# Optimization experiments

Measured on AMD Instinct MI355X. Metric: run time of the kernel, lower is better.

Reference implementation:

```python
import jax, jax.numpy as jnp
import numpy as np

N = 524288   # number of (column, layer) samples
NCH = 30     # n_channel, fixed by the hard-coded filter vectors

# Per-gas channel filters for (h2o, o3, co2, u, n2o, ch4), each length 30.
FILTERS = jnp.array([
    [1,1,1,1,1,1,1,1,1,1,1,1,1,1,1,1,1,1,1,1,1,1,0,0,0,0,0,0,1,1],  # h2o
    [1,1,0,0,0,0,0,0,0,0,0,0,0,0,0,0,1,1,1,1,1,1,0,0,1,1,1,1,1,1],  # o3
    [1,1,0,0,1,1,0,0,1,1,0,0,1,1,0,0,0,0,0,0,0,0,0,0,0,0,0,0,1,1],  # co2
    [1,1,0,0,0,0,0,0,0,0,0,0,0,0,1,1,1,1,1,1,1,1,0,0,0,0,1,1,1,1],  # u
    [1,1,0,0,1,0,0,0,0,0,0,0,0,0,0,0,0,0,0,0,0,0,0,0,0,0,0,0,1,1],  # n2o
    [1,1,1,1,0,0,1,1,0,0,1,1,0,0,0,0,0,0,0,0,0,0,0,0,0,0,0,0,1,1],  # ch4
], dtype=jnp.float32)


def setup_inputs() -> dict:
    key = jax.random.key(0)
    ks = jax.random.split(key, 11)
    u = lambda k, shape, lo, hi: jax.random.uniform(k, shape, jnp.float32, lo, hi)
    return {
        "tpl": jax.random.normal(ks[0], (N, 3), jnp.float32),   # temp, pressure, log_pressure
        "cons": jax.random.uniform(ks[1], (N, 8), jnp.float32), # constituent masses
        # eight Linear(1, 30, bias=False) weights (lw, iw, h2o, o3, co2, u, n2o, ch4)
        "w_gas": u(ks[2], (8, NCH), -0.9, 0.5),
        # six ke-MLPs (2 -> 6 -> 4 -> 4 -> 1), stacked over gas axis g=6
        "ke_W1": u(ks[3], (6, 6, 2), -0.1, 0.1),
        "ke_b1": u(ks[4], (6, 6), 0.9, 1.1),
        "ke_W2": u(ks[5], (6, 4, 6), -0.1, 0.1),
        "ke_b2": u(ks[6], (6, 4), 0.9, 1.1),
        "ke_W3": u(ks[7], (6, 4, 4), -0.1, 0.1),
        "ke_b3": u(ks[8], (6, 4), 0.9, 1.1),
        "ke_Wo": u(ks[9], (6, 4), -0.1, 0.1),
        "ke_bo": u(ks[10], (6,), -0.1, 0.1),
    }


def reference(tpl, cons, w_gas, ke_W1, ke_b1, ke_W2, ke_b2, ke_W3, ke_b3, ke_Wo, ke_bo):
    t_p = tpl[:, :2]                                             # [N,2]
    # six tiny MLPs, vectorized over gas axis g (dropout is identity at eval)
    h = jax.nn.relu(jnp.einsum('ghi,ni->gnh', ke_W1, t_p) + ke_b1[:, None, :])   # [6,N,6]
    h = jax.nn.relu(jnp.einsum('goh,gnh->gno', ke_W2, h) + ke_b2[:, None, :])    # [6,N,4]
    h = jax.nn.relu(jnp.einsum('gph,gnh->gnp', ke_W3, h) + ke_b3[:, None, :])    # [6,N,4]
    s = jax.nn.sigmoid(jnp.einsum('gp,gnp->gn', ke_Wo, h) + ke_bo[:, None])      # [6,N]

    # net_gas(one) == weight vector; exp(w_gas) gives per-channel extinction coeffs
    tau_base = cons[:, None, :] * jnp.exp(w_gas).T[None, :, :]                   # [N,30,8]
    # channel filter * sigmoid modulation for the 6 gas species (slots 2..7)
    mod_gas = (FILTERS[:, None, :] * s[:, :, None]).transpose(1, 2, 0)           # [N,30,6]
    mod = jnp.concatenate(
        [jnp.ones((tpl.shape[0], NCH, 2), tau_base.dtype), mod_gas], axis=2)     # [N,30,8]
    return tau_base * mod                                                        # [N,30,8]
```

## Files before the change

kernel.cpp:

```cpp
#include <hip/hip_runtime.h>
#include <hip/hip_bf16.h>

#define NCHAN 30

__constant__ int FMASK_C[NCHAN] = {63,63,33,33,21,5,33,33,5,5,33,33,5,5,9,9,
                                   11,11,11,11,11,11,0,0,2,2,10,10,63,63};

typedef float f32x4 __attribute__((ext_vector_type(4)));

__global__ __launch_bounds__(256) void ext_kernel(
    const float* __restrict__ tpl,
    const float* __restrict__ cons,
    const float* __restrict__ w_gas,
    const float* __restrict__ W1, const float* __restrict__ b1,
    const float* __restrict__ W2, const float* __restrict__ b2,
    const float* __restrict__ W3, const float* __restrict__ b3,
    const float* __restrict__ Wo, const float* __restrict__ bo,
    f32x4* __restrict__ out4)
{
    __shared__ float p_lds[256][8];
    __shared__ float E_lds[32][8];

    const int tid = threadIdx.x;
    const int n   = blockIdx.x * 256 + tid;

    if (tid < 8 * NCHAN) {
        const int c = tid >> 3, k = tid & 7;
        float e = __expf(w_gas[k * NCHAN + c]);
        if (k >= 2 && !((FMASK_C[c] >> (k - 2)) & 1)) e = 0.f;
        E_lds[c][k] = e;
    }

    const float4* c4 = (const float4*)cons;
    const float4 ca = c4[(size_t)n * 2];
    const float4 cb = c4[(size_t)n * 2 + 1];
    const float t0 = tpl[(size_t)n * 3 + 0];
    const float t1 = tpl[(size_t)n * 3 + 1];

    float s[6];
    #pragma unroll
    for (int g = 0; g < 6; ++g) {
        float h1[6], h2[4], h3[4];
        #pragma unroll
        for (int j = 0; j < 6; ++j)
            h1[j] = fmaxf(0.f, fmaf(W1[g*12 + j*2], t0,
                           fmaf(W1[g*12 + j*2 + 1], t1, b1[g*6 + j])));
        #pragma unroll
        for (int o = 0; o < 4; ++o) {
            float a = b2[g*4 + o];
            #pragma unroll
            for (int j = 0; j < 6; ++j) a = fmaf(W2[g*24 + o*6 + j], h1[j], a);
            h2[o] = fmaxf(0.f, a);
        }
        #pragma unroll
        for (int p = 0; p < 4; ++p) {
            float a = b3[g*4 + p];
            #pragma unroll
            for (int o = 0; o < 4; ++o) a = fmaf(W3[g*16 + p*4 + o], h2[o], a);
            h3[p] = fmaxf(0.f, a);
        }
        float a = bo[g];
        #pragma unroll
        for (int p = 0; p < 4; ++p) a = fmaf(Wo[g*4 + p], h3[p], a);
        s[g] = __fdividef(1.f, 1.f + __expf(-a));
    }

    float4 pa, pb;
    pa.x = ca.x;        pa.y = ca.y;
    pa.z = ca.z * s[0]; pa.w = ca.w * s[1];
    pb.x = cb.x * s[2]; pb.y = cb.y * s[3];
    pb.z = cb.z * s[4]; pb.w = cb.w * s[5];
    *(float4*)&p_lds[tid][0] = pa;
    *(float4*)&p_lds[tid][4] = pb;

    __syncthreads();

    const size_t gbase = (size_t)blockIdx.x * (256 * NCHAN * 2);
    #pragma unroll 6
    for (int i = 0; i < 60; ++i) {
        const unsigned ch  = (unsigned)(i * 256 + tid);
        const unsigned nl  = ch / 60u;
        const unsigned rem = ch - nl * 60u;
        const unsigned c   = rem >> 1;
        const unsigned hi4 = (rem & 1u) << 2;

        const float4 pv = *(const float4*)&p_lds[nl][hi4];
        const float4 ev = *(const float4*)&E_lds[c][hi4];

        f32x4 v;
        v.x = pv.x * ev.x;
        v.y = pv.y * ev.y;
        v.z = pv.z * ev.z;
        v.w = pv.w * ev.w;
        __builtin_nontemporal_store(v, &out4[gbase + ch]);
    }
}

extern "C" void kernel_launch(void* const* d_in, const int* in_sizes, int n_in,
                              void* d_out, int out_size, void* d_ws, size_t ws_size,
                              hipStream_t stream) {
    const float* tpl  = (const float*)d_in[0];
    const float* cons = (const float*)d_in[1];
    const float* wgas = (const float*)d_in[2];
    const float* W1   = (const float*)d_in[3];
    const float* b1   = (const float*)d_in[4];
    const float* W2   = (const float*)d_in[5];
    const float* b2   = (const float*)d_in[6];
    const float* W3   = (const float*)d_in[7];
    const float* b3   = (const float*)d_in[8];
    const float* Wo   = (const float*)d_in[9];
    const float* bo   = (const float*)d_in[10];

    const int nrows = in_sizes[0] / 3;
    const int blocks = nrows / 256;

    ext_kernel<<<dim3(blocks), dim3(256), 0, stream>>>(
        tpl, cons, wgas, W1, b1, W2, b2, W3, b3, Wo, bo, (f32x4*)d_out);
}
```

Baseline: 105.4 us.

## Split fused kernel into MLP pass and separate output-emit pass via workspace

Splits the single fused kernel into two launches. The first computes the per-row modulated constituent vector and the extinction table and writes them to a global workspace. The second reads them back and writes the expanded output. The apparent intent is to separate the compute-heavy MLP phase from the store-bound output phase so each kernel gets better occupancy and no block barrier. The cost is an extra launch and a global-memory round trip of 32 bytes per row.

```diff
diff --git a/kernel.cpp b/kernel.cpp
--- a/kernel.cpp
+++ b/kernel.cpp
@@ -1,5 +1,4 @@
 #include <hip/hip_runtime.h>
-#include <hip/hip_bf16.h>
 
 #define NCHAN 30
 
@@ -8,7 +7,9 @@
 
 typedef float f32x4 __attribute__((ext_vector_type(4)));
 
-__global__ __launch_bounds__(256) void ext_kernel(
+#define WS_P_OFF_F4 64
+
+__global__ __launch_bounds__(256) void mlp_kernel(
     const float* __restrict__ tpl,
     const float* __restrict__ cons,
     const float* __restrict__ w_gas,
@@ -16,19 +17,16 @@
     const float* __restrict__ W2, const float* __restrict__ b2,
     const float* __restrict__ W3, const float* __restrict__ b3,
     const float* __restrict__ Wo, const float* __restrict__ bo,
-    f32x4* __restrict__ out4)
+    float* __restrict__ ws)
 {
-    __shared__ float p_lds[256][8];
-    __shared__ float E_lds[32][8];
-
     const int tid = threadIdx.x;
     const int n   = blockIdx.x * 256 + tid;
 
-    if (tid < 8 * NCHAN) {
+    if (blockIdx.x == 0 && tid < 8 * NCHAN) {
         const int c = tid >> 3, k = tid & 7;
         float e = __expf(w_gas[k * NCHAN + c]);
         if (k >= 2 && !((FMASK_C[c] >> (k - 2)) & 1)) e = 0.f;
-        E_lds[c][k] = e;
+        ws[tid] = e;
     }
 
     const float4* c4 = (const float4*)cons;
@@ -70,22 +68,31 @@
     pa.z = ca.z * s[0]; pa.w = ca.w * s[1];
     pb.x = cb.x * s[2]; pb.y = cb.y * s[3];
     pb.z = cb.z * s[4]; pb.w = cb.w * s[5];
-    *(float4*)&p_lds[tid][0] = pa;
-    *(float4*)&p_lds[tid][4] = pb;
 
-    __syncthreads();
+    float4* p4 = (float4*)ws + WS_P_OFF_F4;
+    p4[(size_t)n * 2]     = pa;
+    p4[(size_t)n * 2 + 1] = pb;
+}
 
-    const size_t gbase = (size_t)blockIdx.x * (256 * NCHAN * 2);
+__global__ __launch_bounds__(256) void emit_kernel(
+    const float* __restrict__ ws,
+    f32x4* __restrict__ out4)
+{
+    const int tid = threadIdx.x;
+    const float4* E4 = (const float4*)ws;
+    const float4* p4 = (const float4*)ws + WS_P_OFF_F4;
+
+    const unsigned rowbase = blockIdx.x * 256u;
+    const size_t   gbase   = (size_t)blockIdx.x * (256 * NCHAN * 2);
+
     #pragma unroll 6
     for (int i = 0; i < 60; ++i) {
         const unsigned ch  = (unsigned)(i * 256 + tid);
         const unsigned nl  = ch / 60u;
         const unsigned rem = ch - nl * 60u;
-        const unsigned c   = rem >> 1;
-        const unsigned hi4 = (rem & 1u) << 2;
 
-        const float4 pv = *(const float4*)&p_lds[nl][hi4];
-        const float4 ev = *(const float4*)&E_lds[c][hi4];
+        const float4 pv = p4[(size_t)(rowbase + nl) * 2 + (rem & 1u)];
+        const float4 ev = E4[rem];
 
         f32x4 v;
         v.x = pv.x * ev.x;
@@ -111,9 +118,14 @@
     const float* Wo   = (const float*)d_in[9];
     const float* bo   = (const float*)d_in[10];
 
-    const int nrows = in_sizes[0] / 3;
+    const int nrows  = in_sizes[0] / 3;
     const int blocks = nrows / 256;
 
-    ext_kernel<<<dim3(blocks), dim3(256), 0, stream>>>(
-        tpl, cons, wgas, W1, b1, W2, b2, W3, b3, Wo, bo, (f32x4*)d_out);
+    float* ws = (float*)d_ws;
+
+    mlp_kernel<<<dim3(blocks), dim3(256), 0, stream>>>(
+        tpl, cons, wgas, W1, b1, W2, b2, W3, b3, Wo, bo, ws);
+
+    emit_kernel<<<dim3(blocks), dim3(256), 0, stream>>>(
+        ws, (f32x4*)d_out);
 }
```

New measurement: 120.7 us. +14.4%, slower.

## Process eight row groups per block with register prefetch and double-buffered LDS

Applied to the files above, without the earlier changes.

Each block now handles eight 256-row groups in a loop instead of one. The next group's cons/tpl loads are issued before the current group's MLP and store phase, and p_lds is double-buffered so only one barrier is needed per group. This amortizes the per-block E table setup and is meant to overlap input latency with compute and the large output stores. The grid shrinks eightfold, to 256 blocks, which may reduce the number of waves available to hide store latency on the device.

```diff
diff --git a/kernel.cpp b/kernel.cpp
--- a/kernel.cpp
+++ b/kernel.cpp
@@ -1,7 +1,7 @@
 #include <hip/hip_runtime.h>
-#include <hip/hip_bf16.h>
 
 #define NCHAN 30
+#define GPB   8
 
 __constant__ int FMASK_C[NCHAN] = {63,63,33,33,21,5,33,33,5,5,33,33,5,5,9,9,
                                    11,11,11,11,11,11,0,0,2,2,10,10,63,63};
@@ -18,11 +18,10 @@
     const float* __restrict__ Wo, const float* __restrict__ bo,
     f32x4* __restrict__ out4)
 {
-    __shared__ float p_lds[256][8];
+    __shared__ float p_lds[2][256][8];
     __shared__ float E_lds[32][8];
 
     const int tid = threadIdx.x;
-    const int n   = blockIdx.x * 256 + tid;
 
     if (tid < 8 * NCHAN) {
         const int c = tid >> 3, k = tid & 7;
@@ -32,67 +31,86 @@
     }
 
     const float4* c4 = (const float4*)cons;
-    const float4 ca = c4[(size_t)n * 2];
-    const float4 cb = c4[(size_t)n * 2 + 1];
-    const float t0 = tpl[(size_t)n * 3 + 0];
-    const float t1 = tpl[(size_t)n * 3 + 1];
 
-    float s[6];
-    #pragma unroll
-    for (int g = 0; g < 6; ++g) {
-        float h1[6], h2[4], h3[4];
+    {
+    }
+    int row = (blockIdx.x * GPB) * 256 + tid;
+    float4 ca = c4[(size_t)row * 2];
+    float4 cb = c4[(size_t)row * 2 + 1];
+    float t0  = tpl[(size_t)row * 3 + 0];
+    float t1  = tpl[(size_t)row * 3 + 1];
+
+    for (int j = 0; j < GPB; ++j) {
+        const int grp = blockIdx.x * GPB + j;
+
+        float4 nca, ncb; float nt0, nt1;
+        if (j + 1 < GPB) {
+            const int nrow = (grp + 1) * 256 + tid;
+            nca = c4[(size_t)nrow * 2];
+            ncb = c4[(size_t)nrow * 2 + 1];
+            nt0 = tpl[(size_t)nrow * 3 + 0];
+            nt1 = tpl[(size_t)nrow * 3 + 1];
+        }
+
+        float s[6];
         #pragma unroll
-        for (int j = 0; j < 6; ++j)
-            h1[j] = fmaxf(0.f, fmaf(W1[g*12 + j*2], t0,
-                           fmaf(W1[g*12 + j*2 + 1], t1, b1[g*6 + j])));
-        #pragma unroll
-        for (int o = 0; o < 4; ++o) {
-            float a = b2[g*4 + o];
+        for (int g = 0; g < 6; ++g) {
+            float h1[6], h2[4], h3[4];
             #pragma unroll
-            for (int j = 0; j < 6; ++j) a = fmaf(W2[g*24 + o*6 + j], h1[j], a);
-            h2[o] = fmaxf(0.f, a);
+            for (int jj = 0; jj < 6; ++jj)
+                h1[jj] = fmaxf(0.f, fmaf(W1[g*12 + jj*2], t0,
+                               fmaf(W1[g*12 + jj*2 + 1], t1, b1[g*6 + jj])));
+            #pragma unroll
+            for (int o = 0; o < 4; ++o) {
+                float a = b2[g*4 + o];
+                #pragma unroll
+                for (int jj = 0; jj < 6; ++jj) a = fmaf(W2[g*24 + o*6 + jj], h1[jj], a);
+                h2[o] = fmaxf(0.f, a);
+            }
+            #pragma unroll
+            for (int p = 0; p < 4; ++p) {
+                float a = b3[g*4 + p];
+                #pragma unroll
+                for (int o = 0; o < 4; ++o) a = fmaf(W3[g*16 + p*4 + o], h2[o], a);
+                h3[p] = fmaxf(0.f, a);
+            }
+            float a = bo[g];
+            #pragma unroll
+            for (int p = 0; p < 4; ++p) a = fmaf(Wo[g*4 + p], h3[p], a);
+            s[g] = __fdividef(1.f, 1.f + __expf(-a));
         }
-        #pragma unroll
-        for (int p = 0; p < 4; ++p) {
-            float a = b3[g*4 + p];
-            #pragma unroll
-            for (int o = 0; o < 4; ++o) a = fmaf(W3[g*16 + p*4 + o], h2[o], a);
-            h3[p] = fmaxf(0.f, a);
+
+        float4 pa, pb;
+        pa.x = ca.x;        pa.y = ca.y;
+        pa.z = ca.z * s[0]; pa.w = ca.w * s[1];
+        pb.x = cb.x * s[2]; pb.y = cb.y * s[3];
+        pb.z = cb.z * s[4]; pb.w = cb.w * s[5];
+        *(float4*)&p_lds[j & 1][tid][0] = pa;
+        *(float4*)&p_lds[j & 1][tid][4] = pb;
+
+        __syncthreads();
+
+        const size_t gbase = (size_t)grp * (256 * NCHAN * 2);
+        const float (* __restrict__ pl)[8] = p_lds[j & 1];
+        #pragma unroll 6
+        for (int i = 0; i < 60; ++i) {
+            const unsigned ch  = (unsigned)(i * 256 + tid);
+            const unsigned nl  = ch / 60u;
+            const unsigned rem = ch - nl * 60u;
+            const unsigned hi4 = (rem & 1u) << 2;
+
+            const float4 pv = *(const float4*)&pl[nl][hi4];
+            const float4 ev = *(const float4*)&E_lds[rem >> 1][hi4];
+
+            f32x4 v;
+            v.x = pv.x * ev.x;
+            v.y = pv.y * ev.y;
+            v.z = pv.z * ev.z;
+            v.w = pv.w * ev.w;
+            __builtin_nontemporal_store(v, &out4[gbase + ch]);
         }
-        float a = bo[g];
-        #pragma unroll
-        for (int p = 0; p < 4; ++p) a = fmaf(Wo[g*4 + p], h3[p], a);
-        s[g] = __fdividef(1.f, 1.f + __expf(-a));
-    }
 
-    float4 pa, pb;
-    pa.x = ca.x;        pa.y = ca.y;
-    pa.z = ca.z * s[0]; pa.w = ca.w * s[1];
-    pb.x = cb.x * s[2]; pb.y = cb.y * s[3];
-    pb.z = cb.z * s[4]; pb.w = cb.w * s[5];
-    *(float4*)&p_lds[tid][0] = pa;
-    *(float4*)&p_lds[tid][4] = pb;
-
-    __syncthreads();
-
-    const size_t gbase = (size_t)blockIdx.x * (256 * NCHAN * 2);
-    #pragma unroll 6
-    for (int i = 0; i < 60; ++i) {
-        const unsigned ch  = (unsigned)(i * 256 + tid);
-        const unsigned nl  = ch / 60u;
-        const unsigned rem = ch - nl * 60u;
-        const unsigned c   = rem >> 1;
-        const unsigned hi4 = (rem & 1u) << 2;
-
-        const float4 pv = *(const float4*)&p_lds[nl][hi4];
-        const float4 ev = *(const float4*)&E_lds[c][hi4];
-
-        f32x4 v;
-        v.x = pv.x * ev.x;
-        v.y = pv.y * ev.y;
-        v.z = pv.z * ev.z;
-        v.w = pv.w * ev.w;
-        __builtin_nontemporal_store(v, &out4[gbase + ch]);
+        ca = nca; cb = ncb; t0 = nt0; t1 = nt1;
     }
 }
 
@@ -111,8 +129,8 @@
     const float* Wo   = (const float*)d_in[9];
     const float* bo   = (const float*)d_in[10];
 
-    const int nrows = in_sizes[0] / 3;
-    const int blocks = nrows / 256;
+    const int nrows  = in_sizes[0] / 3;
+    const int blocks = nrows / (256 * GPB);
 
     ext_kernel<<<dim3(blocks), dim3(256), 0, stream>>>(
         tpl, cons, wgas, W1, b1, W2, b2, W3, b3, Wo, bo, (f32x4*)d_out);
```

Measured after the change: 120.0 us. +13.8%, slower.
